# Optimization experiments

Measured on AMD Instinct MI355X. Metric: run time of the kernel, lower is better.

The kernel has to match this reference:

```python
import jax, jax.numpy as jnp
import numpy as np
from jax import lax

C = 256
HEADS = 8
B = 8
HH = 56
WW = 56
EPS = 1e-5  # BatchNorm2d default eps


def setup_inputs() -> dict:
    key = jax.random.key(0)
    ks = jax.random.split(key, 32)
    i = [0]

    def nxt():
        k = ks[i[0]]
        i[0] += 1
        return k

    def nrm(shape, s=0.05):
        return jax.random.normal(nxt(), shape, jnp.float32) * s

    inp = {
        "x": jax.random.normal(nxt(), (B, HH * WW, C), jnp.float32),
        "H": HH,
        "W": WW,
    }
    for p in ("q", "k", "v"):
        inp[f"{p}_dw_w"] = nrm((C, 1, 3, 3))
        inp[f"{p}_dw_b"] = nrm((C,))
        inp[f"{p}_bn_g"] = jnp.ones((C,), jnp.float32)
        inp[f"{p}_bn_b"] = jnp.zeros((C,), jnp.float32)
        inp[f"{p}_bn_m"] = nrm((C,))
        inp[f"{p}_bn_v"] = jax.random.uniform(nxt(), (C,), jnp.float32)
        inp[f"{p}_pw_w"] = nrm((C, C))
        inp[f"{p}_pw_b"] = nrm((C,))
    inp["proj_w"] = nrm((C, C))
    inp["proj_b"] = nrm((C,))
    return inp


def _sepconv(x4, dw_w, dw_b, g, b, m, v, pw_w, pw_b, stride):
    # depthwise conv (groups=C), NCHW
    y = lax.conv_general_dilated(
        x4, dw_w, (stride, stride), ((1, 1), (1, 1)),
        dimension_numbers=("NCHW", "OIHW", "NCHW"),
        feature_group_count=C,
    ) + dw_b[None, :, None, None]
    # BatchNorm2d (inference: running stats)
    scale = g * lax.rsqrt(v + EPS)
    y = y * scale[None, :, None, None] + (b - m * scale)[None, :, None, None]
    # pointwise 1x1 conv
    y = jnp.einsum("bchw,oc->bohw", y, pw_w) + pw_b[None, :, None, None]
    return y


def reference(x, H, W,
              q_dw_w, q_dw_b, q_bn_g, q_bn_b, q_bn_m, q_bn_v, q_pw_w, q_pw_b,
              k_dw_w, k_dw_b, k_bn_g, k_bn_b, k_bn_m, k_bn_v, k_pw_w, k_pw_b,
              v_dw_w, v_dw_b, v_bn_g, v_bn_b, v_bn_m, v_bn_v, v_pw_w, v_pw_b,
              proj_w, proj_b):
    Bn, N, Cc = x.shape
    d = Cc // HEADS
    scale = d ** -0.5

    # b (l w) c -> b c l w
    x4 = x.reshape(Bn, H, W, Cc).transpose(0, 3, 1, 2)

    q = _sepconv(x4, q_dw_w, q_dw_b, q_bn_g, q_bn_b, q_bn_m, q_bn_v, q_pw_w, q_pw_b, 1)
    k = _sepconv(x4, k_dw_w, k_dw_b, k_bn_g, k_bn_b, k_bn_m, k_bn_v, k_pw_w, k_pw_b, 2)
    v = _sepconv(x4, v_dw_w, v_dw_b, v_bn_g, v_bn_b, v_bn_m, v_bn_v, v_pw_w, v_pw_b, 2)

    # b (h d) l w -> b h (l w) d
    def heads(t):
        b_, c_, h_, w_ = t.shape
        return t.reshape(b_, HEADS, d, h_ * w_).transpose(0, 1, 3, 2)

    qh, kh, vh = heads(q), heads(k), heads(v)

    attn = jnp.einsum("bhid,bhjd->bhij", qh, kh) * scale
    attn = jax.nn.softmax(attn, axis=-1)
    o = jnp.einsum("bhij,bhjd->bhid", attn, vh)
    # b h n d -> b n (h d)
    o = o.transpose(0, 2, 1, 3).reshape(Bn, -1, Cc)
    return o @ proj_w.T + proj_b
```

## Files before the change

kernel.cpp:

```cpp
#include <hip/hip_runtime.h>
#include <hip/hip_bf16.h>
#include <math.h>

#define CI 256
#define BB 8
#define HHH 56
#define WWW 56
#define NN (HHH*WWW)
#define H2 28
#define W2 28
#define N2 (H2*W2)
#define NHEADS 8
#define DDIM 32

typedef __attribute__((ext_vector_type(4))) float  f32x4;
typedef __attribute__((ext_vector_type(8))) short  s16x8;
typedef __attribute__((ext_vector_type(4))) short  s16x4;

#define MFMA32(a,b,c) __builtin_amdgcn_mfma_f32_16x16x32_bf16((a),(b),(c),0,0,0)

#if __has_builtin(__builtin_amdgcn_mfma_f32_16x16x16bf16_1k)
#define MFMA16(a,b,c) __builtin_amdgcn_mfma_f32_16x16x16bf16_1k((a),(b),(c),0,0,0)
#elif __has_builtin(__builtin_amdgcn_mfma_f32_16x16x16_bf16)
#define MFMA16(a,b,c) __builtin_amdgcn_mfma_f32_16x16x16_bf16((a),(b),(c),0,0,0)
#else
static __device__ inline f32x4 mfma16_asm(s16x4 a, s16x4 b, f32x4 c){
    asm volatile("v_mfma_f32_16x16x16_bf16 %0, %1, %2, %0\n\ts_nop 7\n\ts_nop 7"
                 : "+v"(c) : "v"(a), "v"(b));
    return c;
}
#define MFMA16(a,b,c) mfma16_asm((a),(b),(c))
#endif

#if __has_builtin(__builtin_amdgcn_exp2f)
#define EXP2F(x) __builtin_amdgcn_exp2f(x)
#else
#define EXP2F(x) exp2f(x)
#endif

static __device__ inline short f2bf(float x){
    union { __hip_bfloat16 h; short s; } u;
    u.h = __float2bfloat16(x);
    return u.s;
}

#define QSCALE 0.25502989827539787f

__global__ __launch_bounds__(256)
void wcvt4_kernel(const float* __restrict__ s0, const float* __restrict__ s1,
                  const float* __restrict__ s2, const float* __restrict__ s3,
                  __hip_bfloat16* __restrict__ d0, __hip_bfloat16* __restrict__ d1,
                  __hip_bfloat16* __restrict__ d2, __hip_bfloat16* __restrict__ d3,
                  const float* __restrict__ qb_in, float* __restrict__ qb_out)
{
    if (blockIdx.x == 256) {
        qb_out[threadIdx.x] = qb_in[threadIdx.x] * QSCALE;
        return;
    }
    const int which = blockIdx.x >> 6;
    const int i = ((blockIdx.x & 63) * 256 + threadIdx.x) * 4;
    const float* src = (which == 0) ? s0 : (which == 1) ? s1 : (which == 2) ? s2 : s3;
    __hip_bfloat16* dst = (which == 0) ? d0 : (which == 1) ? d1 : (which == 2) ? d2 : d3;
    const float sc = (which == 0) ? QSCALE : 1.0f;
    f32x4 v = *(const f32x4*)(src + i);
    s16x4 o;
    o[0] = f2bf(v[0]*sc); o[1] = f2bf(v[1]*sc); o[2] = f2bf(v[2]*sc); o[3] = f2bf(v[3]*sc);
    *(s16x4*)((short*)dst + i) = o;
}

__global__ __launch_bounds__(256)
void dw_bn3_kernel(const float* __restrict__ x,
                   const float* __restrict__ qw, const float* __restrict__ qwb,
                   const float* __restrict__ qg, const float* __restrict__ qbt,
                   const float* __restrict__ qm, const float* __restrict__ qv,
                   const float* __restrict__ kw, const float* __restrict__ kwb,
                   const float* __restrict__ kg, const float* __restrict__ kbt,
                   const float* __restrict__ km, const float* __restrict__ kv,
                   const float* __restrict__ vw, const float* __restrict__ vwb,
                   const float* __restrict__ vg, const float* __restrict__ vbt,
                   const float* __restrict__ vm, const float* __restrict__ vv,
                   __hip_bfloat16* __restrict__ yq,
                   __hip_bfloat16* __restrict__ yk,
                   __hip_bfloat16* __restrict__ yv)
{
    const int c = threadIdx.x;
    const int p = blockIdx.x;
    const int b = blockIdx.y;
    const int oh = p / WWW, ow = p % WWW;

    float tap[9];
    #pragma unroll
    for (int kh = 0; kh < 3; ++kh) {
        const int ih = oh - 1 + kh;
        #pragma unroll
        for (int kwi = 0; kwi < 3; ++kwi) {
            const int iw = ow - 1 + kwi;
            const bool ok = (ih >= 0) & (ih < HHH) & (iw >= 0) & (iw < WWW);
            tap[kh*3 + kwi] = ok ? x[((size_t)(b*NN + ih*WWW + iw))*CI + c] : 0.0f;
        }
    }

    {
        float acc = qwb[c];
        const float* wc = qw + c*9;
        #pragma unroll
        for (int t = 0; t < 9; ++t) acc += tap[t] * wc[t];
        const float sc = qg[c] * rsqrtf(qv[c] + 1e-5f);
        const float sh = qbt[c] - qm[c]*sc;
        yq[((size_t)(b*NN + p))*CI + c] = __float2bfloat16(acc*sc + sh);
    }

    if (((oh | ow) & 1) == 0) {
        const int p2 = (oh >> 1)*W2 + (ow >> 1);
        {
            float acc = kwb[c];
            const float* wc = kw + c*9;
            #pragma unroll
            for (int t = 0; t < 9; ++t) acc += tap[t] * wc[t];
            const float sc = kg[c] * rsqrtf(kv[c] + 1e-5f);
            const float sh = kbt[c] - km[c]*sc;
            yk[((size_t)(b*N2 + p2))*CI + c] = __float2bfloat16(acc*sc + sh);
        }
        {
            float acc = vwb[c];
            const float* wc = vw + c*9;
            #pragma unroll
            for (int t = 0; t < 9; ++t) acc += tap[t] * wc[t];
            const float sc = vg[c] * rsqrtf(vv[c] + 1e-5f);
            const float sh = vbt[c] - vm[c]*sc;
            yv[((size_t)(b*N2 + p2))*CI + c] = __float2bfloat16(acc*sc + sh);
        }
    }
}

template<bool F32OUT>
__global__ __launch_bounds__(256)
void gemm_kernel(const __hip_bfloat16* __restrict__ A,
                 const __hip_bfloat16* __restrict__ W,
                 const float* __restrict__ bias,
                 void* __restrict__ Cout)
{
    __shared__ short Alds[128][40];
    __shared__ short Blds[128][40];

    const int tid = threadIdx.x;
    const int wave = tid >> 6, lane = tid & 63;
    const int g = lane >> 4, rho = lane & 15;
    const int wr = wave >> 1, wc = wave & 1;
    const int bm = blockIdx.x * 128, bn = blockIdx.y * 128;

    const short* Asrc = (const short*)A;
    const short* Wsrc = (const short*)W;
    const int srow = tid >> 2, sc16 = (tid & 3) * 8;

    f32x4 acc[4][4];
    #pragma unroll
    for (int mt = 0; mt < 4; ++mt)
        #pragma unroll
        for (int nt = 0; nt < 4; ++nt)
            acc[mt][nt] = (f32x4){0.f,0.f,0.f,0.f};

    for (int k0 = 0; k0 < 256; k0 += 32) {
        __syncthreads();
        #pragma unroll
        for (int u = 0; u < 2; ++u) {
            const int row = srow + u*64;
            *(s16x8*)&Alds[row][sc16] =
                *(const s16x8*)(Asrc + (size_t)(bm + row)*256 + k0 + sc16);
            *(s16x8*)&Blds[row][sc16] =
                *(const s16x8*)(Wsrc + (size_t)(bn + row)*256 + k0 + sc16);
        }
        __syncthreads();

        s16x8 af[4], bf_[4];
        #pragma unroll
        for (int mt = 0; mt < 4; ++mt)
            af[mt] = *(const s16x8*)&Alds[wr*64 + mt*16 + rho][g*8];
        #pragma unroll
        for (int nt = 0; nt < 4; ++nt)
            bf_[nt] = *(const s16x8*)&Blds[wc*64 + nt*16 + rho][g*8];
        #pragma unroll
        for (int mt = 0; mt < 4; ++mt)
            #pragma unroll
            for (int nt = 0; nt < 4; ++nt)
                acc[mt][nt] = MFMA32(af[mt], bf_[nt], acc[mt][nt]);
    }

    #pragma unroll
    for (int mt = 0; mt < 4; ++mt)
        #pragma unroll
        for (int nt = 0; nt < 4; ++nt) {
            const int col = bn + wc*64 + nt*16 + rho;
            const float bv = bias[col];
            #pragma unroll
            for (int r = 0; r < 4; ++r) {
                const int row = bm + wr*64 + mt*16 + g*4 + r;
                const float v = acc[mt][nt][r] + bv;
                if (F32OUT) ((float*)Cout)[(size_t)row*256 + col] = v;
                else ((__hip_bfloat16*)Cout)[(size_t)row*256 + col] = __float2bfloat16(v);
            }
        }
}

__global__ __launch_bounds__(256)
void vt_kernel(const __hip_bfloat16* __restrict__ Vb, __hip_bfloat16* __restrict__ VTb)
{
    __shared__ short Vl[16][264];
    const int tid = threadIdx.x;
    const int jb = blockIdx.x * 16, b = blockIdx.y;
    const short* src = (const short*)Vb;
    short* dst = (short*)VTb;

    const int jl = tid >> 4, ch0 = (tid & 15) * 16;
    *(s16x8*)&Vl[jl][ch0]     = *(const s16x8*)(src + (size_t)(b*N2 + jb + jl)*256 + ch0);
    *(s16x8*)&Vl[jl][ch0 + 8] = *(const s16x8*)(src + (size_t)(b*N2 + jb + jl)*256 + ch0 + 8);
    __syncthreads();

    const int chn = tid;
    s16x8 w0, w1;
    #pragma unroll
    for (int u = 0; u < 8; ++u) w0[u] = Vl[u][chn];
    #pragma unroll
    for (int u = 0; u < 8; ++u) w1[u] = Vl[u + 8][chn];
    *(s16x8*)(dst + (size_t)(b*256 + chn)*N2 + jb)     = w0;
    *(s16x8*)(dst + (size_t)(b*256 + chn)*N2 + jb + 8) = w1;
}

__global__ __launch_bounds__(256)
void attn_kernel(const __hip_bfloat16* __restrict__ Qb,
                 const __hip_bfloat16* __restrict__ Kb,
                 const __hip_bfloat16* __restrict__ VTb,
                 __hip_bfloat16* __restrict__ Ob)
{
    __shared__ short Klds[64][40];
    __shared__ short Vlds[32][88];
    __shared__ float Obuf[4][16][40];

    const int tid = threadIdx.x;
    const int wave = tid >> 6, lane = tid & 63;
    const int g = lane >> 4, rho = lane & 15;
    const int bh = blockIdx.y, b = bh >> 3, h = bh & 7;
    const int i0 = blockIdx.x * 64 + wave * 16;

    const s16x8 qf = *(const s16x8*)((const short*)Qb +
                       ((size_t)(b*NN + i0 + rho)*256 + h*DDIM + g*8));

    const int krow = tid >> 2, kc16 = (tid & 3) * 8;
    const int vd = tid >> 3, vj8 = (tid & 7) * 8;
    const short* kptr = (const short*)Kb + ((size_t)(b*N2) + krow)*256 + h*DDIM + kc16;
    const short* vptr = (const short*)VTb + ((size_t)((b*NHEADS + h)*DDIM + vd))*N2 + vj8;

    f32x4 o0 = {0.f,0.f,0.f,0.f}, o1 = {0.f,0.f,0.f,0.f};
    float lsum = 0.f;
    const f32x4 z = {0.f,0.f,0.f,0.f};

    s16x8 kreg = *(const s16x8*)kptr;
    s16x8 vreg = *(const s16x8*)vptr;

    for (int ch = 0; ch < 12; ++ch) {
        __syncthreads();
        *(s16x8*)&Klds[krow][kc16] = kreg;
        *(s16x8*)&Vlds[vd][vj8] = vreg;
        if (ch < 11) {
            kptr += 64*256;  vptr += 64;
            kreg = *(const s16x8*)kptr;
            vreg = *(const s16x8*)vptr;
        }
        __syncthreads();

        f32x4 sarr[4];
        #pragma unroll
        for (int T = 0; T < 4; ++T) {
            const s16x8 kf = *(const s16x8*)&Klds[T*16 + rho][g*8];
            sarr[T] = MFMA32(kf, qf, z);
        }

        #pragma unroll
        for (int T = 0; T < 4; ++T) {
            const float p0 = EXP2F(sarr[T][0]);
            const float p1 = EXP2F(sarr[T][1]);
            const float p2 = EXP2F(sarr[T][2]);
            const float p3 = EXP2F(sarr[T][3]);
            lsum += (p0 + p1) + (p2 + p3);
            s16x4 pb;
            pb[0] = f2bf(p0); pb[1] = f2bf(p1);
            pb[2] = f2bf(p2); pb[3] = f2bf(p3);
            const s16x4 va0 = *(const s16x4*)&Vlds[rho][T*16 + g*4];
            const s16x4 va1 = *(const s16x4*)&Vlds[16 + rho][T*16 + g*4];
            o0 = MFMA16(va0, pb, o0);
            o1 = MFMA16(va1, pb, o1);
        }
    }

    __syncthreads();
    if (tid < 64) {
        const int row = tid >> 2, c16 = (tid & 3) * 8;
        *(s16x8*)&Klds[row][c16] = *(const s16x8*)((const short*)Kb +
            ((size_t)(b*N2 + 768 + row))*256 + h*DDIM + c16);
    } else if (tid < 128) {
        const int t = tid - 64, d = t >> 1, half = (t & 1) * 8;
        *(s16x8*)&Vlds[d][half] = *(const s16x8*)((const short*)VTb +
            ((size_t)((b*NHEADS + h)*DDIM + d))*N2 + 768 + half);
    }
    __syncthreads();
    {
        const s16x8 kf = *(const s16x8*)&Klds[rho][g*8];
        const f32x4 s = MFMA32(kf, qf, z);
        const float p0 = EXP2F(s[0]);
        const float p1 = EXP2F(s[1]);
        const float p2 = EXP2F(s[2]);
        const float p3 = EXP2F(s[3]);
        lsum += (p0 + p1) + (p2 + p3);
        s16x4 pb;
        pb[0] = f2bf(p0); pb[1] = f2bf(p1);
        pb[2] = f2bf(p2); pb[3] = f2bf(p3);
        const s16x4 va0 = *(const s16x4*)&Vlds[rho][g*4];
        const s16x4 va1 = *(const s16x4*)&Vlds[16 + rho][g*4];
        o0 = MFMA16(va0, pb, o0);
        o1 = MFMA16(va1, pb, o1);
    }

    lsum += __shfl_xor(lsum, 16);
    lsum += __shfl_xor(lsum, 32);
    const float inv = 1.0f / lsum;

    #pragma unroll
    for (int r = 0; r < 4; ++r) {
        Obuf[wave][rho][g*4 + r]      = o0[r] * inv;
        Obuf[wave][rho][16 + g*4 + r] = o1[r] * inv;
    }
    asm volatile("s_waitcnt lgkmcnt(0)" ::: "memory");

    const int q = lane >> 2, d0 = (lane & 3) * 8;
    const f32x4 a  = *(const f32x4*)&Obuf[wave][q][d0];
    const f32x4 a2 = *(const f32x4*)&Obuf[wave][q][d0 + 4];
    s16x8 w;
    w[0] = f2bf(a[0]);  w[1] = f2bf(a[1]);  w[2] = f2bf(a[2]);  w[3] = f2bf(a[3]);
    w[4] = f2bf(a2[0]); w[5] = f2bf(a2[1]); w[6] = f2bf(a2[2]); w[7] = f2bf(a2[3]);
    *(s16x8*)((short*)Ob + ((size_t)(b*NN + i0 + q)*256 + h*DDIM + d0)) = w;
}

extern "C" void kernel_launch(void* const* d_in, const int* in_sizes, int n_in,
                              void* d_out, int out_size, void* d_ws, size_t ws_size,
                              hipStream_t stream)
{
    const float* x      = (const float*)d_in[0];
    const float* q_dw_w = (const float*)d_in[3];
    const float* q_dw_b = (const float*)d_in[4];
    const float* q_bn_g = (const float*)d_in[5];
    const float* q_bn_b = (const float*)d_in[6];
    const float* q_bn_m = (const float*)d_in[7];
    const float* q_bn_v = (const float*)d_in[8];
    const float* q_pw_w = (const float*)d_in[9];
    const float* q_pw_b = (const float*)d_in[10];
    const float* k_dw_w = (const float*)d_in[11];
    const float* k_dw_b = (const float*)d_in[12];
    const float* k_bn_g = (const float*)d_in[13];
    const float* k_bn_b = (const float*)d_in[14];
    const float* k_bn_m = (const float*)d_in[15];
    const float* k_bn_v = (const float*)d_in[16];
    const float* k_pw_w = (const float*)d_in[17];
    const float* k_pw_b = (const float*)d_in[18];
    const float* v_dw_w = (const float*)d_in[19];
    const float* v_dw_b = (const float*)d_in[20];
    const float* v_bn_g = (const float*)d_in[21];
    const float* v_bn_b = (const float*)d_in[22];
    const float* v_bn_m = (const float*)d_in[23];
    const float* v_bn_v = (const float*)d_in[24];
    const float* v_pw_w = (const float*)d_in[25];
    const float* v_pw_b = (const float*)d_in[26];
    const float* proj_w = (const float*)d_in[27];
    const float* proj_b = (const float*)d_in[28];

    __hip_bfloat16* p = (__hip_bfloat16*)d_ws;
    __hip_bfloat16* yq  = p;  p += (size_t)BB*NN*CI;
    __hip_bfloat16* yk  = p;  p += (size_t)BB*N2*CI;
    __hip_bfloat16* yv  = p;  p += (size_t)BB*N2*CI;
    __hip_bfloat16* Qb  = p;  p += (size_t)BB*NN*CI;
    __hip_bfloat16* Kb  = p;  p += (size_t)BB*N2*CI;
    __hip_bfloat16* Vb  = p;  p += (size_t)BB*N2*CI;
    __hip_bfloat16* VTb = p;  p += (size_t)BB*N2*CI;
    __hip_bfloat16* wq  = p;  p += (size_t)CI*CI;
    __hip_bfloat16* wk  = p;  p += (size_t)CI*CI;
    __hip_bfloat16* wv  = p;  p += (size_t)CI*CI;
    __hip_bfloat16* wpj = p;  p += (size_t)CI*CI;
    float* qb_scaled = (float*)p;
    __hip_bfloat16* Ob  = yq;

    wcvt4_kernel<<<257, 256, 0, stream>>>(q_pw_w, k_pw_w, v_pw_w, proj_w,
                                          wq, wk, wv, wpj, q_pw_b, qb_scaled);

    dw_bn3_kernel<<<dim3(NN, BB), 256, 0, stream>>>(
        x,
        q_dw_w, q_dw_b, q_bn_g, q_bn_b, q_bn_m, q_bn_v,
        k_dw_w, k_dw_b, k_bn_g, k_bn_b, k_bn_m, k_bn_v,
        v_dw_w, v_dw_b, v_bn_g, v_bn_b, v_bn_m, v_bn_v,
        yq, yk, yv);

    gemm_kernel<false><<<dim3(BB*NN/128, 2), 256, 0, stream>>>(yq, wq, qb_scaled, Qb);
    gemm_kernel<false><<<dim3(BB*N2/128, 2), 256, 0, stream>>>(yk, wk, k_pw_b, Kb);
    gemm_kernel<false><<<dim3(BB*N2/128, 2), 256, 0, stream>>>(yv, wv, v_pw_b, Vb);

    vt_kernel<<<dim3(N2/16, BB), 256, 0, stream>>>(Vb, VTb);

    attn_kernel<<<dim3(NN/64, BB*NHEADS), 256, 0, stream>>>(Qb, Kb, VTb, Ob);

    gemm_kernel<true><<<dim3(BB*NN/128, 2), 256, 0, stream>>>(Ob, wpj, proj_b, d_out);
}
```

Before: 260.1 us.

## Fuse K/V GEMMs with transposed V epilogue, prefetch GEMM tiles, swizzle blocks

Merges the K and V pointwise GEMMs into one launch whose V path writes head-transposed output directly, eliminating the separate transpose kernel and the intermediate V buffer. GEMM main loops now prefetch the next K-slice into registers before the MFMA phase to overlap global loads. The depthwise and attention kernels remap block indices to interleave batches/heads, and the attention probability packing uses a cheaper add-and-permute bf16 conversion with round-half-up instead of round-to-nearest-even, slightly changing rounding.

```diff
diff --git a/kernel.cpp b/kernel.cpp
--- a/kernel.cpp
+++ b/kernel.cpp
@@ -42,6 +42,16 @@
     union { __hip_bfloat16 h; short s; } u;
     u.h = __float2bfloat16(x);
     return u.s;
+}
+
+static __device__ inline unsigned pack_bf16_rhu(float a, float b){
+    const unsigned ua = __float_as_uint(a) + 0x8000u;
+    const unsigned ub = __float_as_uint(b) + 0x8000u;
+#if __has_builtin(__builtin_amdgcn_perm)
+    return __builtin_amdgcn_perm(ub, ua, 0x07060302u);
+#else
+    return (ub & 0xFFFF0000u) | (ua >> 16);
+#endif
 }
 
 #define QSCALE 0.25502989827539787f
@@ -84,8 +94,9 @@
                    __hip_bfloat16* __restrict__ yv)
 {
     const int c = threadIdx.x;
-    const int p = blockIdx.x;
-    const int b = blockIdx.y;
+    const int lin = blockIdx.y * NN + blockIdx.x;
+    const int b = lin & 7;
+    const int p = lin >> 3;
     const int oh = p / WWW, ow = p % WWW;
 
     float tap[9];
@@ -133,7 +144,7 @@
     }
 }
 
-template<bool F32OUT>
+template<int OUTMODE>
 __global__ __launch_bounds__(256)
 void gemm_kernel(const __hip_bfloat16* __restrict__ A,
                  const __hip_bfloat16* __restrict__ W,
@@ -149,9 +160,12 @@
     const int wr = wave >> 1, wc = wave & 1;
     const int bm = blockIdx.x * 128, bn = blockIdx.y * 128;
 
-    const short* Asrc = (const short*)A;
-    const short* Wsrc = (const short*)W;
     const int srow = tid >> 2, sc16 = (tid & 3) * 8;
+    const short* Ap = (const short*)A + (size_t)(bm + srow)*256 + sc16;
+    const short* Wp = (const short*)W + (size_t)(bn + srow)*256 + sc16;
+
+    s16x8 a0 = *(const s16x8*)Ap, a1 = *(const s16x8*)(Ap + 64*256);
+    s16x8 b0 = *(const s16x8*)Wp, b1 = *(const s16x8*)(Wp + 64*256);
 
     f32x4 acc[4][4];
     #pragma unroll
@@ -162,13 +176,14 @@
 
     for (int k0 = 0; k0 < 256; k0 += 32) {
         __syncthreads();
-        #pragma unroll
-        for (int u = 0; u < 2; ++u) {
-            const int row = srow + u*64;
-            *(s16x8*)&Alds[row][sc16] =
-                *(const s16x8*)(Asrc + (size_t)(bm + row)*256 + k0 + sc16);
-            *(s16x8*)&Blds[row][sc16] =
-                *(const s16x8*)(Wsrc + (size_t)(bn + row)*256 + k0 + sc16);
+        *(s16x8*)&Alds[srow][sc16]      = a0;
+        *(s16x8*)&Alds[srow + 64][sc16] = a1;
+        *(s16x8*)&Blds[srow][sc16]      = b0;
+        *(s16x8*)&Blds[srow + 64][sc16] = b1;
+        if (k0 < 224) {
+            Ap += 32; Wp += 32;
+            a0 = *(const s16x8*)Ap; a1 = *(const s16x8*)(Ap + 64*256);
+            b0 = *(const s16x8*)Wp; b1 = *(const s16x8*)(Wp + 64*256);
         }
         __syncthreads();
 
@@ -196,34 +211,108 @@
             for (int r = 0; r < 4; ++r) {
                 const int row = bm + wr*64 + mt*16 + g*4 + r;
                 const float v = acc[mt][nt][r] + bv;
-                if (F32OUT) ((float*)Cout)[(size_t)row*256 + col] = v;
+                if (OUTMODE == 1) ((float*)Cout)[(size_t)row*256 + col] = v;
                 else ((__hip_bfloat16*)Cout)[(size_t)row*256 + col] = __float2bfloat16(v);
             }
         }
 }
 
 __global__ __launch_bounds__(256)
-void vt_kernel(const __hip_bfloat16* __restrict__ Vb, __hip_bfloat16* __restrict__ VTb)
+void gemm_kv_kernel(const __hip_bfloat16* __restrict__ Ak,
+                    const __hip_bfloat16* __restrict__ Av,
+                    const __hip_bfloat16* __restrict__ Wk,
+                    const __hip_bfloat16* __restrict__ Wv,
+                    const float* __restrict__ biask,
+                    const float* __restrict__ biasv,
+                    __hip_bfloat16* __restrict__ Kb,
+                    __hip_bfloat16* __restrict__ VTb)
 {
-    __shared__ short Vl[16][264];
+    __shared__ short Alds[128][40];
+    __shared__ short Blds[128][40];
+
     const int tid = threadIdx.x;
-    const int jb = blockIdx.x * 16, b = blockIdx.y;
-    const short* src = (const short*)Vb;
-    short* dst = (short*)VTb;
-
-    const int jl = tid >> 4, ch0 = (tid & 15) * 16;
-    *(s16x8*)&Vl[jl][ch0]     = *(const s16x8*)(src + (size_t)(b*N2 + jb + jl)*256 + ch0);
-    *(s16x8*)&Vl[jl][ch0 + 8] = *(const s16x8*)(src + (size_t)(b*N2 + jb + jl)*256 + ch0 + 8);
-    __syncthreads();
-
-    const int chn = tid;
-    s16x8 w0, w1;
+    const int wave = tid >> 6, lane = tid & 63;
+    const int g = lane >> 4, rho = lane & 15;
+    const int wr = wave >> 1, wc = wave & 1;
+    const int bm = blockIdx.x * 128, bn = blockIdx.y * 128;
+    const int isv = blockIdx.z;
+
+    const short* Asrc = (const short*)(isv ? Av : Ak);
+    const short* Wsrc = (const short*)(isv ? Wv : Wk);
+    const float* bias = isv ? biasv : biask;
+
+    const int srow = tid >> 2, sc16 = (tid & 3) * 8;
+    const short* Ap = Asrc + (size_t)(bm + srow)*256 + sc16;
+    const short* Wp = Wsrc + (size_t)(bn + srow)*256 + sc16;
+
+    s16x8 a0 = *(const s16x8*)Ap, a1 = *(const s16x8*)(Ap + 64*256);
+    s16x8 b0 = *(const s16x8*)Wp, b1 = *(const s16x8*)(Wp + 64*256);
+
+    f32x4 acc[4][4];
     #pragma unroll
-    for (int u = 0; u < 8; ++u) w0[u] = Vl[u][chn];
-    #pragma unroll
-    for (int u = 0; u < 8; ++u) w1[u] = Vl[u + 8][chn];
-    *(s16x8*)(dst + (size_t)(b*256 + chn)*N2 + jb)     = w0;
-    *(s16x8*)(dst + (size_t)(b*256 + chn)*N2 + jb + 8) = w1;
+    for (int mt = 0; mt < 4; ++mt)
+        #pragma unroll
+        for (int nt = 0; nt < 4; ++nt)
+            acc[mt][nt] = (f32x4){0.f,0.f,0.f,0.f};
+
+    for (int k0 = 0; k0 < 256; k0 += 32) {
+        __syncthreads();
+        *(s16x8*)&Alds[srow][sc16]      = a0;
+        *(s16x8*)&Alds[srow + 64][sc16] = a1;
+        *(s16x8*)&Blds[srow][sc16]      = b0;
+        *(s16x8*)&Blds[srow + 64][sc16] = b1;
+        if (k0 < 224) {
+            Ap += 32; Wp += 32;
+            a0 = *(const s16x8*)Ap; a1 = *(const s16x8*)(Ap + 64*256);
+            b0 = *(const s16x8*)Wp; b1 = *(const s16x8*)(Wp + 64*256);
+        }
+        __syncthreads();
+
+        s16x8 af[4], bf_[4];
+        #pragma unroll
+        for (int mt = 0; mt < 4; ++mt)
+            af[mt] = *(const s16x8*)&Alds[wr*64 + mt*16 + rho][g*8];
+        #pragma unroll
+        for (int nt = 0; nt < 4; ++nt)
+            bf_[nt] = *(const s16x8*)&Blds[wc*64 + nt*16 + rho][g*8];
+        #pragma unroll
+        for (int mt = 0; mt < 4; ++mt)
+            #pragma unroll
+            for (int nt = 0; nt < 4; ++nt)
+                acc[mt][nt] = MFMA32(af[mt], bf_[nt], acc[mt][nt]);
+    }
+
+    if (!isv) {
+        #pragma unroll
+        for (int mt = 0; mt < 4; ++mt)
+            #pragma unroll
+            for (int nt = 0; nt < 4; ++nt) {
+                const int col = bn + wc*64 + nt*16 + rho;
+                const float bv = bias[col];
+                #pragma unroll
+                for (int r = 0; r < 4; ++r) {
+                    const int row = bm + wr*64 + mt*16 + g*4 + r;
+                    Kb[(size_t)row*256 + col] = __float2bfloat16(acc[mt][nt][r] + bv);
+                }
+            }
+    } else {
+        #pragma unroll
+        for (int mt = 0; mt < 4; ++mt)
+            #pragma unroll
+            for (int nt = 0; nt < 4; ++nt) {
+                const int col = bn + wc*64 + nt*16 + rho;
+                const float bv = bias[col];
+                const int row0 = bm + wr*64 + mt*16 + g*4;
+                const int bb = row0 / N2;
+                const int j0 = row0 - bb*N2;
+                s16x4 o4;
+                #pragma unroll
+                for (int r = 0; r < 4; ++r)
+                    o4[r] = f2bf(acc[mt][nt][r] + bv);
+                *(s16x4*)((short*)VTb +
+                    ((size_t)(bb*NHEADS + (col >> 5))*DDIM + (col & 31))*N2 + j0) = o4;
+            }
+    }
 }
 
 __global__ __launch_bounds__(256)
@@ -239,8 +328,13 @@
     const int tid = threadIdx.x;
     const int wave = tid >> 6, lane = tid & 63;
     const int g = lane >> 4, rho = lane & 15;
-    const int bh = blockIdx.y, b = bh >> 3, h = bh & 7;
-    const int i0 = blockIdx.x * 64 + wave * 16;
+
+    const int lin = blockIdx.y * 49 + blockIdx.x;
+    const int swz = (lin & 7) * 392 + (lin >> 3);
+    const int iblk = swz % 49;
+    const int bh = swz / 49;
+    const int b = bh >> 3, h = bh & 7;
+    const int i0 = iblk * 64 + wave * 16;
 
     const s16x8 qf = *(const s16x8*)((const short*)Qb +
                        ((size_t)(b*NN + i0 + rho)*256 + h*DDIM + g*8));
@@ -282,13 +376,13 @@
             const float p2 = EXP2F(sarr[T][2]);
             const float p3 = EXP2F(sarr[T][3]);
             lsum += (p0 + p1) + (p2 + p3);
-            s16x4 pb;
-            pb[0] = f2bf(p0); pb[1] = f2bf(p1);
-            pb[2] = f2bf(p2); pb[3] = f2bf(p3);
+            union { unsigned u[2]; s16x4 v; } pk;
+            pk.u[0] = pack_bf16_rhu(p0, p1);
+            pk.u[1] = pack_bf16_rhu(p2, p3);
             const s16x4 va0 = *(const s16x4*)&Vlds[rho][T*16 + g*4];
             const s16x4 va1 = *(const s16x4*)&Vlds[16 + rho][T*16 + g*4];
-            o0 = MFMA16(va0, pb, o0);
-            o1 = MFMA16(va1, pb, o1);
+            o0 = MFMA16(va0, pk.v, o0);
+            o1 = MFMA16(va1, pk.v, o1);
         }
     }
 
@@ -311,13 +405,13 @@
         const float p2 = EXP2F(s[2]);
         const float p3 = EXP2F(s[3]);
         lsum += (p0 + p1) + (p2 + p3);
-        s16x4 pb;
-        pb[0] = f2bf(p0); pb[1] = f2bf(p1);
-        pb[2] = f2bf(p2); pb[3] = f2bf(p3);
+        union { unsigned u[2]; s16x4 v; } pk;
+        pk.u[0] = pack_bf16_rhu(p0, p1);
+        pk.u[1] = pack_bf16_rhu(p2, p3);
         const s16x4 va0 = *(const s16x4*)&Vlds[rho][g*4];
         const s16x4 va1 = *(const s16x4*)&Vlds[16 + rho][g*4];
-        o0 = MFMA16(va0, pb, o0);
-        o1 = MFMA16(va1, pb, o1);
+        o0 = MFMA16(va0, pk.v, o0);
+        o1 = MFMA16(va1, pk.v, o1);
     }
 
     lsum += __shfl_xor(lsum, 16);
@@ -378,7 +472,6 @@
     __hip_bfloat16* yv  = p;  p += (size_t)BB*N2*CI;
     __hip_bfloat16* Qb  = p;  p += (size_t)BB*NN*CI;
     __hip_bfloat16* Kb  = p;  p += (size_t)BB*N2*CI;
-    __hip_bfloat16* Vb  = p;  p += (size_t)BB*N2*CI;
     __hip_bfloat16* VTb = p;  p += (size_t)BB*N2*CI;
     __hip_bfloat16* wq  = p;  p += (size_t)CI*CI;
     __hip_bfloat16* wk  = p;  p += (size_t)CI*CI;
@@ -397,13 +490,12 @@
         v_dw_w, v_dw_b, v_bn_g, v_bn_b, v_bn_m, v_bn_v,
         yq, yk, yv);
 
-    gemm_kernel<false><<<dim3(BB*NN/128, 2), 256, 0, stream>>>(yq, wq, qb_scaled, Qb);
-    gemm_kernel<false><<<dim3(BB*N2/128, 2), 256, 0, stream>>>(yk, wk, k_pw_b, Kb);
-    gemm_kernel<false><<<dim3(BB*N2/128, 2), 256, 0, stream>>>(yv, wv, v_pw_b, Vb);
-
-    vt_kernel<<<dim3(N2/16, BB), 256, 0, stream>>>(Vb, VTb);
+    gemm_kernel<0><<<dim3(BB*NN/128, 2), 256, 0, stream>>>(yq, wq, qb_scaled, Qb);
+
+    gemm_kv_kernel<<<dim3(BB*N2/128, 2, 2), 256, 0, stream>>>(
+        yk, yv, wk, wv, k_pw_b, v_pw_b, Kb, VTb);
 
     attn_kernel<<<dim3(NN/64, BB*NHEADS), 256, 0, stream>>>(Qb, Kb, VTb, Ob);
 
-    gemm_kernel<true><<<dim3(BB*NN/128, 2), 256, 0, stream>>>(Ob, wpj, proj_b, d_out);
-}
+    gemm_kernel<1><<<dim3(BB*NN/128, 2), 256, 0, stream>>>(Ob, wpj, proj_b, d_out);
+}
```

Result: faster. 227.1 us (-12.7%).
